# Kernel optimization log

Measured on AMD Instinct MI355X. Metric: run time of the kernel, lower is better.

Reference implementation:

```python
import jax, jax.numpy as jnp
import numpy as np
import math

# dims: batch, in-channels, freq bins, frames(=cropsize), ffn dim, bands
B, C, BINS, W, FF, NB = 16, 8, 1024, 256, 2048, 4
EPS = 1e-5


def _ln(x, g, b):
    m = x.mean(-1, keepdims=True)
    v = ((x - m) ** 2).mean(-1, keepdims=True)
    return (x - m) / jnp.sqrt(v + EPS) * g + b


def _conv1d(x, w, groups=1):
    # x: [b, Cin, L], w: [Cout, Cin//groups, K], 'same' padding
    pad = (w.shape[-1] - 1) // 2
    return jax.lax.conv_general_dilated(
        x, w, (1,), [(pad, pad)],
        dimension_numbers=('NCH', 'OIH', 'NCH'), feature_group_count=groups)


def _mb_attn(x, mem, qw, qb, kw, kb, vw, vb, ow, ob, er, dist_w):
    # MultibandFrameAttention with skewed relative-position bias
    b, w, c = x.shape
    d = c // NB
    q = (x @ qw.T + qb).reshape(b, w, NB, d).transpose(0, 2, 1, 3)    # [b,nb,w,d]
    k = (mem @ kw.T + kb).reshape(b, w, NB, d).transpose(0, 2, 3, 1)  # [b,nb,d,w]
    v = (mem @ vw.T + vb).reshape(b, w, NB, d).transpose(0, 2, 1, 3)  # [b,nb,w,d]
    # skew trick: q @ er -> pad left on last dim -> transpose -> drop first row
    qer = jnp.einsum('bnwd,dc->bnwc', q, er)                           # [b,nb,w,W]
    skew = jnp.pad(qer, ((0, 0), (0, 0), (0, 0), (1, 0)))
    skew = skew.transpose(0, 1, 3, 2)[:, :, 1:, :]                     # [b,nb,W,w]
    idx = jnp.arange(w)
    dist = jnp.abs(idx[:, None] - idx[None, :]).astype(x.dtype) / 2.0  # [w,w]
    p = dist[None] * dist_w + skew                                     # [b,nb,w,w]
    qk = jnp.einsum('bnwd,bndk->bnwk', q, k) / math.sqrt(c)
    a = jax.nn.softmax(qk + p, axis=-1)
    o = jnp.einsum('bnwk,bnkd->bnwd', a, v).transpose(0, 2, 1, 3).reshape(b, w, c)
    return o @ ow.T + ob


def setup_inputs() -> dict:
    key = jax.random.key(0)
    ks = jax.random.split(key, 24)
    rn = lambda k, s, sc=0.02: jax.random.normal(k, s, dtype=jnp.float32) * sc
    d = BINS // NB
    ones = lambda n: jnp.ones((n,), jnp.float32)
    zeros = lambda n: jnp.zeros((n,), jnp.float32)
    return {
        'x': jax.random.normal(ks[0], (B, C, BINS, W), jnp.float32),
        'bott_w': rn(ks[1], (1, C), 0.3),
        'bn_g': ones(1), 'bn_b': zeros(1), 'bn_m': zeros(1), 'bn_v': ones(1),
        'glu_w': rn(ks[2], (2 * BINS, BINS)),
        'n1g': ones(BINS), 'n1b': zeros(BINS),
        'c1L_w': rn(ks[3], (2 * FF, BINS)),
        'c1R_w': rn(ks[4], (FF // 2, BINS, 3)),
        'n2g': ones(2 * FF), 'n2b': zeros(2 * FF),
        'c2dw_w': rn(ks[5], (2 * FF, 1, 9), 0.1),
        'c2pw_w': rn(ks[6], (FF // 2, 2 * FF)),
        'n3g': ones(BINS), 'n3b': zeros(BINS),
        'qw': rn(ks[7], (BINS, BINS)), 'qb': zeros(BINS),
        'kw': rn(ks[8], (BINS, BINS)), 'kb': zeros(BINS),
        'vw': rn(ks[9], (BINS, BINS)), 'vb': zeros(BINS),
        'ow': rn(ks[10], (BINS, BINS)), 'ob': zeros(BINS),
        'er': rn(ks[11], (d, W), 0.02),
        'dist_w': rn(ks[12], (NB, W, 1), 0.02),
        'n4g': ones(BINS), 'n4b': zeros(BINS),
        'c3_w': rn(ks[13], (2 * FF, BINS)),
        'c4_w': rn(ks[14], (BINS, 2 * FF)),
        'n5g': ones(BINS), 'n5b': zeros(BINS),
    }


def reference(x, bott_w, bn_g, bn_b, bn_m, bn_v, glu_w, n1g, n1b,
              c1L_w, c1R_w, n2g, n2b, c2dw_w, c2pw_w, n3g, n3b,
              qw, qb, kw, kb, vw, vb, ow, ob, er, dist_w,
              n4g, n4b, c3_w, c4_w, n5g, n5b):
    # bottleneck: Linear(C->1) over channel dim, BatchNorm2d(1) eval, ReLU
    h0 = jnp.einsum('bchw,oc->bohw', x, bott_w)                        # [b,1,bins,w]
    h0 = (h0 - bn_m[None, :, None, None]) / jnp.sqrt(bn_v[None, :, None, None] + EPS)
    h0 = jax.nn.relu(h0 * bn_g[None, :, None, None] + bn_b[None, :, None, None])
    xs = h0[:, 0].transpose(0, 2, 1)                                   # [b,w,bins]

    # GLU block
    g = xs @ glu_w.T
    a, bgate = g[..., :BINS], g[..., BINS:]
    xs = _ln(xs + a * jax.nn.sigmoid(bgate), n1g, n1b)

    # conv/linear FFN
    hL = jax.nn.relu(xs @ c1L_w.T)                                     # [b,w,2ff]
    hR = jax.nn.relu(_conv1d(xs.transpose(0, 2, 1), c1R_w).transpose(0, 2, 1))
    hR = jnp.pad(hR, ((0, 0), (0, 0), (0, hL.shape[2] - hR.shape[2])))
    h = _ln(hL + hR, n2g, n2b)
    t = _conv1d(h.transpose(0, 2, 1), c2dw_w, groups=2 * FF)           # depthwise
    t = jnp.einsum('bcl,oc->bol', t, c2pw_w).transpose(0, 2, 1)        # [b,w,ff//2]
    t = jnp.pad(t, ((0, 0), (0, 0), (0, xs.shape[2] - t.shape[2])))
    xs = _ln(xs + t, n3g, n3b)

    # multiband attention (self)
    h = _mb_attn(xs, xs, qw, qb, kw, kb, vw, vb, ow, ob, er, dist_w)
    xs = _ln(xs + h, n4g, n4b)

    # final FFN
    h = jax.nn.relu(xs @ c3_w.T) @ c4_w.T
    xs = _ln(xs + h, n5g, n5b)
    return xs.transpose(0, 2, 1)[:, None]                              # [b,1,bins,w]
```

## Files before the change

kernel.cpp:

```cpp
#include <hip/hip_runtime.h>
#include <hip/hip_bf16.h>

#define EPSF 1e-5f

typedef unsigned short u16;
typedef unsigned int   u32;
typedef __attribute__((ext_vector_type(8))) short bf16x8;
typedef __attribute__((ext_vector_type(4))) float f32x4;

__device__ __forceinline__ u16 f2bf(float f) {
    u32 u = __builtin_bit_cast(u32, f);
    u32 r = u + 0x7fffu + ((u >> 16) & 1u);
    return (u16)(r >> 16);
}
__device__ __forceinline__ float bf2f(u16 h) {
    return __builtin_bit_cast(float, (u32)h << 16);
}
__device__ __forceinline__ void gld16(void* lds, const void* gsrc) {
    __builtin_amdgcn_global_load_lds(
        (const __attribute__((address_space(1))) u32*)gsrc,
        (__attribute__((address_space(3))) u32*)lds, 16, 0, 0);
}

__device__ __forceinline__ float wred_sum(float v) {
#pragma unroll
    for (int off = 32; off; off >>= 1) v += __shfl_xor(v, off, 64);
    return v;
}
__device__ __forceinline__ void block_red2(float& s1, float& s2, int tid) {
    __shared__ float red[8];
    s1 = wred_sum(s1); s2 = wred_sum(s2);
    const int lane = tid & 63, wid = tid >> 6;
    if (!lane) { red[wid] = s1; red[4 + wid] = s2; }
    __syncthreads();
    s1 = red[0] + red[1] + red[2] + red[3];
    s2 = red[4] + red[5] + red[6] + red[7];
}

struct Cvt9 { const float* s[9]; u16* d[9]; int n[9]; };
__global__ __launch_bounds__(256)
void wcvt9_k(Cvt9 a)
{
    const int seg = blockIdx.y;
    const int i = blockIdx.x * 256 + threadIdx.x;
    if (i >= a.n[seg]) return;
    const float4 v = ((const float4*)a.s[seg])[i];
    ushort4 o; o.x = f2bf(v.x); o.y = f2bf(v.y); o.z = f2bf(v.z); o.w = f2bf(v.w);
    ((ushort4*)a.d[seg])[i] = o;
}
__global__ __launch_bounds__(256)
void c1rcvt_k(const float* __restrict__ src, u16* __restrict__ dst)
{
    const int i = blockIdx.x * 256 + threadIdx.x;
    const int q = i / 3072, rem = i - q * 3072;
    const int ks = rem >> 10, ci = rem & 1023;
    dst[i] = f2bf(src[((long)q * 1024 + ci) * 3 + ks]);
}
__global__ __launch_bounds__(256)
void ercvt_k(const float* __restrict__ er, u16* __restrict__ erT)
{
    const int i = blockIdx.x * 256 + threadIdx.x;
    const int c = i >> 8, d = i & 255;
    erT[i] = f2bf(er[d * 256 + c]);
}
__global__ __launch_bounds__(256)
void dwcvt_k(const float* __restrict__ src, float* __restrict__ dst)
{
    const int i = blockIdx.x * 256 + threadIdx.x;
    if (i >= 9 * 4096) return;
    const int k = i >> 12, c = i & 4095;
    dst[i] = src[c * 9 + k];
}
__global__ __launch_bounds__(256)
void zero_k(u16* __restrict__ p, int n)
{
    const int i = blockIdx.x * 256 + threadIdx.x;
    if (i < n) p[i] = 0;
}
__global__ __launch_bounds__(256)
void biascat_k(const float* __restrict__ b0, const float* __restrict__ b1,
               const float* __restrict__ b2, float* __restrict__ dst)
{
    const int i = blockIdx.x * 256 + threadIdx.x;
    const float* s = (i < 1024) ? b0 : ((i < 2048) ? b1 : b2);
    dst[i] = s[i & 1023];
}

__global__ __launch_bounds__(256)
void bottleneck_k(const float* __restrict__ x, const float* __restrict__ bw,
                  const float* __restrict__ bn_g, const float* __restrict__ bn_b,
                  const float* __restrict__ bn_m, const float* __restrict__ bn_v,
                  float* __restrict__ xs, u16* __restrict__ xsb)
{
    __shared__ float tile[32][33];
    const int b = blockIdx.z, h0 = blockIdx.y * 32, w0 = blockIdx.x * 32;
    const int tid = threadIdx.x, c = tid & 31, r = tid >> 5;
    float wreg[8];
#pragma unroll
    for (int ch = 0; ch < 8; ++ch) wreg[ch] = bw[ch];
    const float sc = bn_g[0] * rsqrtf(bn_v[0] + EPSF);
    const float sh = bn_b[0] - bn_m[0] * sc;
#pragma unroll
    for (int it = 0; it < 4; ++it) {
        const int h = h0 + r + it * 8;
        const int w = w0 + c;
        float acc = 0.f;
#pragma unroll
        for (int ch = 0; ch < 8; ++ch)
            acc += x[(((long)b * 8 + ch) * 1024 + h) * 256 + w] * wreg[ch];
        tile[r + it * 8][c] = fmaxf(acc * sc + sh, 0.f);
    }
    __syncthreads();
#pragma unroll
    for (int it = 0; it < 4; ++it) {
        const int wl = r + it * 8;
        const float v = tile[c][wl];
        const long o = ((long)b * 256 + w0 + wl) * 1024 + h0 + c;
        xs[o] = v;
        xsb[o] = f2bf(v);
    }
}

template<int ACT, int OUTBF, int BIAS, int SPLITK>
__global__ __launch_bounds__(512, 2)
void gemm8_k(const u16* __restrict__ A, const u16* __restrict__ B,
             const float* __restrict__ bias, void* __restrict__ Cout,
             int N, int K , int lda, int ldb, long partStride)
{
    extern __shared__ u16 lds[];
    const int m0 = blockIdx.y * 256, n0 = blockIdx.x * 256;
    const int koff = (SPLITK > 1) ? blockIdx.z * K : 0;
    const int nt = K >> 6;
    const int tid = threadIdx.x;
    const int lane = tid & 63, wid = tid >> 6;
    const int wr = ((wid >> 2) & 1) * 128;
    const int wc = (wid & 3) * 64;
    const int l15 = lane & 15, l4 = lane >> 4;

    const u16* Ag = A + (long)m0 * lda + koff;
    const u16* Bg = B + (long)n0 * ldb + koff;

    auto stage = [&](const u16* g, int ld, int ldsbase, int kcol, int h) {
#pragma unroll
        for (int is = 0; is < 2; ++is) {
            const int r = h * 128 + is * 64 + (tid >> 3);
            const int sc = ((tid & 7) * 8) ^ (((r >> 2) & 1) << 4);
            gld16(&lds[ldsbase + h * 8192 + is * 4096 + tid * 8],
                  g + (long)r * ld + kcol + sc);
        }
    };
    auto frag = [&](int base, int row, int col) -> bf16x8 {
        return *(const bf16x8*)&lds[base + row * 64 + (col ^ (((row >> 2) & 1) << 4))];
    };

    f32x4 acc[8][4] = {};

    stage(Ag, lda, 0, 0, 0);
    stage(Ag, lda, 0, 0, 1);
    stage(Bg, ldb, 32768, 0, 0);
    stage(Bg, ldb, 32768, 0, 1);
    if (nt > 1) {
        stage(Bg, ldb, 49152, 64, 0);
        stage(Bg, ldb, 49152, 64, 1);
        stage(Ag, lda, 16384, 64, 0);
        asm volatile("s_waitcnt vmcnt(6)" ::: "memory");
    } else {
        asm volatile("s_waitcnt vmcnt(0)" ::: "memory");
    }
    __builtin_amdgcn_s_barrier();

    for (int kt = 0; kt < nt; ++kt) {
        const int cs = kt & 1;
        const int ab = cs * 16384;
        const int bb = 32768 + cs * 16384;
        const int abn = (cs ^ 1) * 16384;
        const int kc1 = (kt + 1) * 64, kc2 = (kt + 2) * 64;
        bf16x8 alo[4][2], ahi[4][2], b01[2][2], b23[2][2];

#pragma unroll
        for (int i = 0; i < 4; ++i)
#pragma unroll
            for (int kk = 0; kk < 2; ++kk)
                alo[i][kk] = frag(ab, wr + i * 16 + l15, kk * 32 + l4 * 8);
#pragma unroll
        for (int j = 0; j < 2; ++j)
#pragma unroll
            for (int kk = 0; kk < 2; ++kk)
                b01[j][kk] = frag(bb, wc + j * 16 + l15, kk * 32 + l4 * 8);
        if (kt + 1 < nt) stage(Ag, lda, abn, kc1, 1);
        __builtin_amdgcn_s_barrier();
        asm volatile("s_waitcnt lgkmcnt(0)" ::: "memory");
        __builtin_amdgcn_s_setprio(1);
#pragma unroll
        for (int i = 0; i < 4; ++i)
#pragma unroll
            for (int j = 0; j < 2; ++j)
#pragma unroll
                for (int kk = 0; kk < 2; ++kk)
                    acc[i][j] = __builtin_amdgcn_mfma_f32_16x16x32_bf16(alo[i][kk], b01[j][kk], acc[i][j], 0, 0, 0);
        __builtin_amdgcn_s_setprio(0);
        __builtin_amdgcn_s_barrier();

#pragma unroll
        for (int j = 0; j < 2; ++j)
#pragma unroll
            for (int kk = 0; kk < 2; ++kk)
                b23[j][kk] = frag(bb, wc + (j + 2) * 16 + l15, kk * 32 + l4 * 8);
        if (kt + 2 < nt) stage(Bg, ldb, bb, kc2, 0);
        __builtin_amdgcn_s_barrier();
        asm volatile("s_waitcnt lgkmcnt(0)" ::: "memory");
        __builtin_amdgcn_s_setprio(1);
#pragma unroll
        for (int i = 0; i < 4; ++i)
#pragma unroll
            for (int j = 0; j < 2; ++j)
#pragma unroll
                for (int kk = 0; kk < 2; ++kk)
                    acc[i][j + 2] = __builtin_amdgcn_mfma_f32_16x16x32_bf16(alo[i][kk], b23[j][kk], acc[i][j + 2], 0, 0, 0);
        __builtin_amdgcn_s_setprio(0);
        __builtin_amdgcn_s_barrier();

#pragma unroll
        for (int i = 0; i < 4; ++i)
#pragma unroll
            for (int kk = 0; kk < 2; ++kk)
                ahi[i][kk] = frag(ab, wr + (i + 4) * 16 + l15, kk * 32 + l4 * 8);
        if (kt + 2 < nt) stage(Bg, ldb, bb, kc2, 1);
        __builtin_amdgcn_s_barrier();
        asm volatile("s_waitcnt lgkmcnt(0)" ::: "memory");
        __builtin_amdgcn_s_setprio(1);
#pragma unroll
        for (int i = 0; i < 4; ++i)
#pragma unroll
            for (int j = 0; j < 2; ++j)
#pragma unroll
                for (int kk = 0; kk < 2; ++kk)
                    acc[i + 4][j + 2] = __builtin_amdgcn_mfma_f32_16x16x32_bf16(ahi[i][kk], b23[j][kk], acc[i + 4][j + 2], 0, 0, 0);
        __builtin_amdgcn_s_setprio(0);
        __builtin_amdgcn_s_barrier();

        if (kt + 2 < nt) stage(Ag, lda, ab, kc2, 0);
        __builtin_amdgcn_s_barrier();
        __builtin_amdgcn_s_setprio(1);
#pragma unroll
        for (int i = 0; i < 4; ++i)
#pragma unroll
            for (int j = 0; j < 2; ++j)
#pragma unroll
                for (int kk = 0; kk < 2; ++kk)
                    acc[i + 4][j] = __builtin_amdgcn_mfma_f32_16x16x32_bf16(ahi[i][kk], b01[j][kk], acc[i + 4][j], 0, 0, 0);
        __builtin_amdgcn_s_setprio(0);
        if (kt + 2 < nt) {
            asm volatile("s_waitcnt vmcnt(6)" ::: "memory");
        } else {
            asm volatile("s_waitcnt vmcnt(0)" ::: "memory");
        }
        __builtin_amdgcn_s_barrier();
    }

    float* Cf = (float*)Cout + ((SPLITK > 1) ? (long)blockIdx.z * partStride : 0);
    u16*   Cb = (u16*)Cout;
#pragma unroll
    for (int i = 0; i < 8; ++i)
#pragma unroll
        for (int j = 0; j < 4; ++j) {
            const int n = n0 + wc + j * 16 + l15;
            const float bv = BIAS ? bias[n] : 0.f;
#pragma unroll
            for (int q = 0; q < 4; ++q) {
                const int m = m0 + wr + i * 16 + l4 * 4 + q;
                float v = acc[i][j][q] + bv;
                if (ACT) v = fmaxf(v, 0.f);
                if (OUTBF) Cb[(long)m * N + n] = f2bf(v);
                else       Cf[(long)m * N + n] = v;
            }
        }
}

__global__ __launch_bounds__(512, 2)
void conv38_k(const u16* __restrict__ Xb, const u16* __restrict__ Wt,
              const u16* __restrict__ zp, float* __restrict__ C)
{
    extern __shared__ u16 lds[];
    const int ks = blockIdx.z;
    const int m0 = blockIdx.y * 256, n0 = blockIdx.x * 256;
    const int nt = 16;
    const int tid = threadIdx.x;
    const int lane = tid & 63, wid = tid >> 6;
    const int wr = ((wid >> 2) & 1) * 128;
    const int wc = (wid & 3) * 64;
    const int l15 = lane & 15, l4 = lane >> 4;

    auto stageA = [&](int ldsbase, int kcol, int h) {
#pragma unroll
        for (int is = 0; is < 2; ++is) {
            const int r = h * 128 + is * 64 + (tid >> 3);
            const int sc = ((tid & 7) * 8) ^ (((r >> 2) & 1) << 4);
            const int t = m0 + r;
            const int wp = (t & 255) + ks - 1;
            const u16* src = ((unsigned)wp < 256u)
                ? Xb + (long)(t + ks - 1) * 1024 + kcol + sc
                : zp;
            gld16(&lds[ldsbase + h * 8192 + is * 4096 + tid * 8], src);
        }
    };
    auto stageB = [&](int ldsbase, int kcol, int h) {
#pragma unroll
        for (int is = 0; is < 2; ++is) {
            const int r = h * 128 + is * 64 + (tid >> 3);
            const int sc = ((tid & 7) * 8) ^ (((r >> 2) & 1) << 4);
            gld16(&lds[ldsbase + h * 8192 + is * 4096 + tid * 8],
                  Wt + (long)(n0 + r) * 3072 + ks * 1024 + kcol + sc);
        }
    };
    auto frag = [&](int base, int row, int col) -> bf16x8 {
        return *(const bf16x8*)&lds[base + row * 64 + (col ^ (((row >> 2) & 1) << 4))];
    };

    f32x4 acc[8][4] = {};

    stageA(0, 0, 0);
    stageA(0, 0, 1);
    stageB(32768, 0, 0);
    stageB(32768, 0, 1);
    stageB(49152, 64, 0);
    stageB(49152, 64, 1);
    stageA(16384, 64, 0);
    asm volatile("s_waitcnt vmcnt(6)" ::: "memory");
    __builtin_amdgcn_s_barrier();

    for (int kt = 0; kt < nt; ++kt) {
        const int cs = kt & 1;
        const int ab = cs * 16384;
        const int bb = 32768 + cs * 16384;
        const int abn = (cs ^ 1) * 16384;
        const int kc1 = (kt + 1) * 64, kc2 = (kt + 2) * 64;
        bf16x8 alo[4][2], ahi[4][2], b01[2][2], b23[2][2];

#pragma unroll
        for (int i = 0; i < 4; ++i)
#pragma unroll
            for (int kk = 0; kk < 2; ++kk)
                alo[i][kk] = frag(ab, wr + i * 16 + l15, kk * 32 + l4 * 8);
#pragma unroll
        for (int j = 0; j < 2; ++j)
#pragma unroll
            for (int kk = 0; kk < 2; ++kk)
                b01[j][kk] = frag(bb, wc + j * 16 + l15, kk * 32 + l4 * 8);
        if (kt + 1 < nt) stageA(abn, kc1, 1);
        __builtin_amdgcn_s_barrier();
        asm volatile("s_waitcnt lgkmcnt(0)" ::: "memory");
        __builtin_amdgcn_s_setprio(1);
#pragma unroll
        for (int i = 0; i < 4; ++i)
#pragma unroll
            for (int j = 0; j < 2; ++j)
#pragma unroll
                for (int kk = 0; kk < 2; ++kk)
                    acc[i][j] = __builtin_amdgcn_mfma_f32_16x16x32_bf16(alo[i][kk], b01[j][kk], acc[i][j], 0, 0, 0);
        __builtin_amdgcn_s_setprio(0);
        __builtin_amdgcn_s_barrier();

#pragma unroll
        for (int j = 0; j < 2; ++j)
#pragma unroll
            for (int kk = 0; kk < 2; ++kk)
                b23[j][kk] = frag(bb, wc + (j + 2) * 16 + l15, kk * 32 + l4 * 8);
        if (kt + 2 < nt) stageB(bb, kc2, 0);
        __builtin_amdgcn_s_barrier();
        asm volatile("s_waitcnt lgkmcnt(0)" ::: "memory");
        __builtin_amdgcn_s_setprio(1);
#pragma unroll
        for (int i = 0; i < 4; ++i)
#pragma unroll
            for (int j = 0; j < 2; ++j)
#pragma unroll
                for (int kk = 0; kk < 2; ++kk)
                    acc[i][j + 2] = __builtin_amdgcn_mfma_f32_16x16x32_bf16(alo[i][kk], b23[j][kk], acc[i][j + 2], 0, 0, 0);
        __builtin_amdgcn_s_setprio(0);
        __builtin_amdgcn_s_barrier();

#pragma unroll
        for (int i = 0; i < 4; ++i)
#pragma unroll
            for (int kk = 0; kk < 2; ++kk)
                ahi[i][kk] = frag(ab, wr + (i + 4) * 16 + l15, kk * 32 + l4 * 8);
        if (kt + 2 < nt) stageB(bb, kc2, 1);
        __builtin_amdgcn_s_barrier();
        asm volatile("s_waitcnt lgkmcnt(0)" ::: "memory");
        __builtin_amdgcn_s_setprio(1);
#pragma unroll
        for (int i = 0; i < 4; ++i)
#pragma unroll
            for (int j = 0; j < 2; ++j)
#pragma unroll
                for (int kk = 0; kk < 2; ++kk)
                    acc[i + 4][j + 2] = __builtin_amdgcn_mfma_f32_16x16x32_bf16(ahi[i][kk], b23[j][kk], acc[i + 4][j + 2], 0, 0, 0);
        __builtin_amdgcn_s_setprio(0);
        __builtin_amdgcn_s_barrier();

        if (kt + 2 < nt) stageA(ab, kc2, 0);
        __builtin_amdgcn_s_barrier();
        __builtin_amdgcn_s_setprio(1);
#pragma unroll
        for (int i = 0; i < 4; ++i)
#pragma unroll
            for (int j = 0; j < 2; ++j)
#pragma unroll
                for (int kk = 0; kk < 2; ++kk)
                    acc[i + 4][j] = __builtin_amdgcn_mfma_f32_16x16x32_bf16(ahi[i][kk], b01[j][kk], acc[i + 4][j], 0, 0, 0);
        __builtin_amdgcn_s_setprio(0);
        if (kt + 2 < nt) {
            asm volatile("s_waitcnt vmcnt(6)" ::: "memory");
        } else {
            asm volatile("s_waitcnt vmcnt(0)" ::: "memory");
        }
        __builtin_amdgcn_s_barrier();
    }

    float* Cp = C + (long)ks * 4194304;
#pragma unroll
    for (int i = 0; i < 8; ++i)
#pragma unroll
        for (int j = 0; j < 4; ++j) {
            const int n = n0 + wc + j * 16 + l15;
#pragma unroll
            for (int q = 0; q < 4; ++q) {
                const int m = m0 + wr + i * 16 + l4 * 4 + q;
                Cp[(long)m * 1024 + n] = acc[i][j][q];
            }
        }
}

__global__ __launch_bounds__(256, 2)
void attn_fused_k(const u16* __restrict__ QKVb, const u16* __restrict__ erT,
                  const u16* __restrict__ Vt, const float* __restrict__ dwp,
                  u16* __restrict__ Oc)
{
    __shared__ __align__(16) u16 As[4096];
    __shared__ __align__(16) u16 Bs[16384];
    __shared__ __align__(16) u16 Pl[16384];
    __shared__ float redM[4][64];
    __shared__ float redS[4][64];
    const int z = blockIdx.y, zb = z >> 2, zn = z & 3;
    const int m0 = blockIdx.x * 64;
    const int tid = threadIdx.x;
    const int lane = tid & 63, wid = tid >> 6;
    const int l15 = lane & 15, l4 = lane >> 4;

    const u16* Qg = QKVb + (long)(zb * 256) * 3072 + zn * 256;
    const u16* Kg = Qg + 1024;

    auto stageA64 = [&](const u16* g, long ld) {
#pragma unroll
        for (int p = 0; p < 2; ++p) {
            const int e = p * 2048 + tid * 8;
            const int r = e >> 6, c = e & 63;
            const int sc = c ^ (((r >> 2) & 1) << 4);
            gld16(&As[e], g + (long)r * ld + sc);
        }
    };
    auto stageB256 = [&](const u16* g, long ld) {
#pragma unroll
        for (int p = 0; p < 8; ++p) {
            const int e = p * 2048 + tid * 8;
            const int r = e >> 6, c = e & 63;
            const int sc = c ^ (((r >> 2) & 1) << 4);
            gld16(&Bs[e], g + (long)r * ld + sc);
        }
    };
    auto fragA = [&](int i, int kk) -> bf16x8 {
        const int row = i * 16 + l15, col = kk * 32 + l4 * 8;
        return *(const bf16x8*)&As[row * 64 + (col ^ (((row >> 2) & 1) << 4))];
    };
    auto fragB = [&](int j, int kk) -> bf16x8 {
        const int row = wid * 64 + j * 16 + l15, col = kk * 32 + l4 * 8;
        return *(const bf16x8*)&Bs[row * 64 + (col ^ (((row >> 2) & 1) << 4))];
    };
    auto fragP = [&](int kc, int i, int kk) -> bf16x8 {
        const int row = i * 16 + l15, col = kk * 32 + l4 * 8;
        return *(const bf16x8*)&Pl[kc * 4096 + row * 64 + (col ^ (((row >> 2) & 1) << 4))];
    };

    f32x4 acc1[4][4] = {};
    f32x4 acc2[4][4] = {};

    for (int kc = 0; kc < 4; ++kc) {
        __syncthreads();
        stageA64(Qg + (long)m0 * 3072 + kc * 64, 3072);
        stageB256(Kg + kc * 64, 3072);
        __syncthreads();
#pragma unroll
        for (int i = 0; i < 4; ++i) {
            const bf16x8 a0 = fragA(i, 0), a1 = fragA(i, 1);
#pragma unroll
            for (int j = 0; j < 4; ++j) {
                acc1[i][j] = __builtin_amdgcn_mfma_f32_16x16x32_bf16(a0, fragB(j, 0), acc1[i][j], 0, 0, 0);
                acc1[i][j] = __builtin_amdgcn_mfma_f32_16x16x32_bf16(a1, fragB(j, 1), acc1[i][j], 0, 0, 0);
            }
        }
    }
    for (int kc = 0; kc < 4; ++kc) {
        __syncthreads();
        stageA64(erT + (long)m0 * 256 + kc * 64, 256);
        stageB256(Qg + kc * 64, 3072);
        __syncthreads();
#pragma unroll
        for (int i = 0; i < 4; ++i) {
            const bf16x8 a0 = fragA(i, 0), a1 = fragA(i, 1);
#pragma unroll
            for (int j = 0; j < 4; ++j) {
                acc2[i][j] = __builtin_amdgcn_mfma_f32_16x16x32_bf16(a0, fragB(j, 0), acc2[i][j], 0, 0, 0);
                acc2[i][j] = __builtin_amdgcn_mfma_f32_16x16x32_bf16(a1, fragB(j, 1), acc2[i][j], 0, 0, 0);
            }
        }
    }

    const float inv32 = 1.f / 32.f;
#pragma unroll
    for (int i = 0; i < 4; ++i)
#pragma unroll
        for (int q = 0; q < 4; ++q) {
            const int mg = m0 + i * 16 + l4 * 4 + q;
            const float dw = dwp[zn * 256 + mg];
#pragma unroll
            for (int j = 0; j < 4; ++j) {
                const int ng = wid * 64 + j * 16 + l15;
                acc1[i][j][q] = acc1[i][j][q] * inv32 + acc2[i][j][q]
                              + fabsf((float)(mg - ng)) * 0.5f * dw;
            }
        }

    float rmax[4][4], rsum[4][4];
#pragma unroll
    for (int i = 0; i < 4; ++i)
#pragma unroll
        for (int q = 0; q < 4; ++q) {
            float mv = fmaxf(fmaxf(acc1[i][0][q], acc1[i][1][q]),
                             fmaxf(acc1[i][2][q], acc1[i][3][q]));
#pragma unroll
            for (int off = 1; off <= 8; off <<= 1) mv = fmaxf(mv, __shfl_xor(mv, off, 64));
            rmax[i][q] = mv;
        }
    if (l15 == 0) {
#pragma unroll
        for (int i = 0; i < 4; ++i)
#pragma unroll
            for (int q = 0; q < 4; ++q)
                redM[wid][i * 16 + l4 * 4 + q] = rmax[i][q];
    }
    __syncthreads();
#pragma unroll
    for (int i = 0; i < 4; ++i)
#pragma unroll
        for (int q = 0; q < 4; ++q) {
            const int ml = i * 16 + l4 * 4 + q;
            rmax[i][q] = fmaxf(fmaxf(redM[0][ml], redM[1][ml]), fmaxf(redM[2][ml], redM[3][ml]));
        }
#pragma unroll
    for (int i = 0; i < 4; ++i)
#pragma unroll
        for (int q = 0; q < 4; ++q) {
            float sv = 0.f;
#pragma unroll
            for (int j = 0; j < 4; ++j) {
                const float e = __expf(acc1[i][j][q] - rmax[i][q]);
                acc1[i][j][q] = e;
                sv += e;
            }
#pragma unroll
            for (int off = 1; off <= 8; off <<= 1) sv += __shfl_xor(sv, off, 64);
            rsum[i][q] = sv;
        }
    if (l15 == 0) {
#pragma unroll
        for (int i = 0; i < 4; ++i)
#pragma unroll
            for (int q = 0; q < 4; ++q)
                redS[wid][i * 16 + l4 * 4 + q] = rsum[i][q];
    }
    __syncthreads();
#pragma unroll
    for (int i = 0; i < 4; ++i)
#pragma unroll
        for (int q = 0; q < 4; ++q) {
            const int ml = i * 16 + l4 * 4 + q;
            rsum[i][q] = redS[0][ml] + redS[1][ml] + redS[2][ml] + redS[3][ml];
        }
#pragma unroll
    for (int i = 0; i < 4; ++i)
#pragma unroll
        for (int q = 0; q < 4; ++q) {
            const float rinv = 1.f / rsum[i][q];
            const int ml = i * 16 + l4 * 4 + q;
#pragma unroll
            for (int j = 0; j < 4; ++j) {
                const int nc = j * 16 + l15;
                Pl[wid * 4096 + ml * 64 + (nc ^ (((ml >> 2) & 1) << 4))] = f2bf(acc1[i][j][q] * rinv);
            }
        }
    __syncthreads();

    f32x4 accO[4][4] = {};
    for (int kc = 0; kc < 4; ++kc) {
        __syncthreads();
        stageB256(Vt + (long)(z * 256) * 256 + kc * 64, 256);
        __syncthreads();
#pragma unroll
        for (int i = 0; i < 4; ++i) {
            const bf16x8 a0 = fragP(kc, i, 0), a1 = fragP(kc, i, 1);
#pragma unroll
            for (int j = 0; j < 4; ++j) {
                accO[i][j] = __builtin_amdgcn_mfma_f32_16x16x32_bf16(a0, fragB(j, 0), accO[i][j], 0, 0, 0);
                accO[i][j] = __builtin_amdgcn_mfma_f32_16x16x32_bf16(a1, fragB(j, 1), accO[i][j], 0, 0, 0);
            }
        }
    }

#pragma unroll
    for (int i = 0; i < 4; ++i)
#pragma unroll
        for (int j = 0; j < 4; ++j) {
            const int d = wid * 64 + j * 16 + l15;
#pragma unroll
            for (int q = 0; q < 4; ++q) {
                const int mg = m0 + i * 16 + l4 * 4 + q;
                Oc[(long)(zb * 256 + mg) * 1024 + zn * 256 + d] = f2bf(accO[i][j][q]);
            }
        }
}

__global__ __launch_bounds__(256)
void glu_ln_k(const float* __restrict__ xs0, const float* __restrict__ g2,
              const float* __restrict__ gam, const float* __restrict__ bet,
              float* __restrict__ outf, u16* __restrict__ outb)
{
    const int t = blockIdx.x, tid = threadIdx.x;
    const int f0 = tid * 4;
    const long PS = 8388608;
    const float4 xv = *(const float4*)&xs0[(long)t * 1024 + f0];
    float4 av = *(const float4*)&g2[(long)t * 2048 + f0];
    float4 gv = *(const float4*)&g2[(long)t * 2048 + 1024 + f0];
    const float4 av1 = *(const float4*)&g2[PS + (long)t * 2048 + f0];
    const float4 gv1 = *(const float4*)&g2[PS + (long)t * 2048 + 1024 + f0];
    av.x += av1.x; av.y += av1.y; av.z += av1.z; av.w += av1.w;
    gv.x += gv1.x; gv.y += gv1.y; gv.z += gv1.z; gv.w += gv1.w;
    float vals[4];
    vals[0] = xv.x + av.x / (1.f + expf(-gv.x));
    vals[1] = xv.y + av.y / (1.f + expf(-gv.y));
    vals[2] = xv.z + av.z / (1.f + expf(-gv.z));
    vals[3] = xv.w + av.w / (1.f + expf(-gv.w));
    float s1 = vals[0] + vals[1] + vals[2] + vals[3];
    float s2 = vals[0]*vals[0] + vals[1]*vals[1] + vals[2]*vals[2] + vals[3]*vals[3];
    block_red2(s1, s2, tid);
    const float mean = s1 * (1.f / 1024.f);
    const float var  = s2 * (1.f / 1024.f) - mean * mean;
    const float rstd = rsqrtf(var + EPSF);
    const float4 gm = *(const float4*)&gam[f0];
    const float4 bt = *(const float4*)&bet[f0];
    float r0 = (vals[0] - mean) * rstd * gm.x + bt.x;
    float r1 = (vals[1] - mean) * rstd * gm.y + bt.y;
    float r2 = (vals[2] - mean) * rstd * gm.z + bt.z;
    float r3 = (vals[3] - mean) * rstd * gm.w + bt.w;
    *(float4*)&outf[(long)t * 1024 + f0] = make_float4(r0, r1, r2, r3);
    ushort4 ub; ub.x = f2bf(r0); ub.y = f2bf(r1); ub.z = f2bf(r2); ub.w = f2bf(r3);
    *(ushort4*)&outb[(long)t * 1024 + f0] = ub;
}

template<int P, int WRITEBF, int BIAS>
__global__ __launch_bounds__(256)
void add_ln1024_k(const float* __restrict__ A, const float* __restrict__ Bp,
                  const float* __restrict__ bias,
                  const float* __restrict__ gam, const float* __restrict__ bet,
                  float* __restrict__ outf, u16* __restrict__ outb)
{
    const int t = blockIdx.x, tid = threadIdx.x;
    const int f0 = tid * 4;
    const long PS = 4194304;
    const float4 a = *(const float4*)&A[(long)t * 1024 + f0];
    float4 b = *(const float4*)&Bp[(long)t * 1024 + f0];
#pragma unroll
    for (int p = 1; p < P; ++p) {
        const float4 bp = *(const float4*)&Bp[p * PS + (long)t * 1024 + f0];
        b.x += bp.x; b.y += bp.y; b.z += bp.z; b.w += bp.w;
    }
    if (BIAS) {
        const float4 bb = *(const float4*)&bias[f0];
        b.x += bb.x; b.y += bb.y; b.z += bb.z; b.w += bb.w;
    }
    float vals[4] = {a.x + b.x, a.y + b.y, a.z + b.z, a.w + b.w};
    float s1 = vals[0] + vals[1] + vals[2] + vals[3];
    float s2 = vals[0]*vals[0] + vals[1]*vals[1] + vals[2]*vals[2] + vals[3]*vals[3];
    block_red2(s1, s2, tid);
    const float mean = s1 * (1.f / 1024.f);
    const float var  = s2 * (1.f / 1024.f) - mean * mean;
    const float rstd = rsqrtf(var + EPSF);
    const float4 gm = *(const float4*)&gam[f0];
    const float4 bt = *(const float4*)&bet[f0];
    float r0 = (vals[0] - mean) * rstd * gm.x + bt.x;
    float r1 = (vals[1] - mean) * rstd * gm.y + bt.y;
    float r2 = (vals[2] - mean) * rstd * gm.z + bt.z;
    float r3 = (vals[3] - mean) * rstd * gm.w + bt.w;
    *(float4*)&outf[(long)t * 1024 + f0] = make_float4(r0, r1, r2, r3);
    if (WRITEBF) {
        ushort4 ub; ub.x = f2bf(r0); ub.y = f2bf(r1); ub.z = f2bf(r2); ub.w = f2bf(r3);
        *(ushort4*)&outb[(long)t * 1024 + f0] = ub;
    }
}

__global__ __launch_bounds__(256)
void add_ln4096_k(const u16* __restrict__ A, const float* __restrict__ Bp,
                  const float* __restrict__ gam, const float* __restrict__ bet,
                  u16* __restrict__ outb)
{
    const int t = blockIdx.x, tid = threadIdx.x;
    const long PS = 4194304;
    const int f0 = tid * 16;
    float vals[16];
    const bf16x8 a0 = *(const bf16x8*)&A[(long)t * 4096 + f0];
    const bf16x8 a1 = *(const bf16x8*)&A[(long)t * 4096 + f0 + 8];
#pragma unroll
    for (int e = 0; e < 8; ++e) { vals[e] = bf2f((u16)a0[e]); vals[8 + e] = bf2f((u16)a1[e]); }
    if (tid < 64) {
#pragma unroll
        for (int c = 0; c < 4; ++c) {
            const int fc = f0 + c * 4;
            float4 b  = *(const float4*)&Bp[(long)t * 1024 + fc];
            const float4 b1 = *(const float4*)&Bp[PS + (long)t * 1024 + fc];
            const float4 b2 = *(const float4*)&Bp[2 * PS + (long)t * 1024 + fc];
            vals[c*4+0] += fmaxf(b.x + b1.x + b2.x, 0.f);
            vals[c*4+1] += fmaxf(b.y + b1.y + b2.y, 0.f);
            vals[c*4+2] += fmaxf(b.z + b1.z + b2.z, 0.f);
            vals[c*4+3] += fmaxf(b.w + b1.w + b2.w, 0.f);
        }
    }
    float s1 = 0.f, s2 = 0.f;
#pragma unroll
    for (int e = 0; e < 16; ++e) { s1 += vals[e]; s2 += vals[e] * vals[e]; }
    block_red2(s1, s2, tid);
    const float mean = s1 * (1.f / 4096.f);
    const float var  = s2 * (1.f / 4096.f) - mean * mean;
    const float rstd = rsqrtf(var + EPSF);
#pragma unroll
    for (int c = 0; c < 4; ++c) {
        const int fc = f0 + c * 4;
        const float4 gm = *(const float4*)&gam[fc];
        const float4 bt = *(const float4*)&bet[fc];
        ushort4 ub;
        ub.x = f2bf((vals[c*4+0] - mean) * rstd * gm.x + bt.x);
        ub.y = f2bf((vals[c*4+1] - mean) * rstd * gm.y + bt.y);
        ub.z = f2bf((vals[c*4+2] - mean) * rstd * gm.z + bt.z);
        ub.w = f2bf((vals[c*4+3] - mean) * rstd * gm.w + bt.w);
        *(ushort4*)&outb[(long)t * 4096 + fc] = ub;
    }
}

__global__ __launch_bounds__(256)
void dwconv8_k(const u16* __restrict__ h, const float* __restrict__ wT,
               u16* __restrict__ out)
{
    const long idx = (long)blockIdx.x * 256 + threadIdx.x;
    const int cg = (int)(idx & 511);
    const int t  = (int)(idx >> 9);
    const int w  = t & 255;
    const int c0 = cg * 8;
    float acc[8] = {};
#pragma unroll
    for (int k = 0; k < 9; ++k) {
        const int wp = w + k - 4;
        if ((unsigned)wp < 256u) {
            const bf16x8 hv = *(const bf16x8*)&h[(long)(t + k - 4) * 4096 + c0];
            const float4 w0 = *(const float4*)&wT[k * 4096 + c0];
            const float4 w1 = *(const float4*)&wT[k * 4096 + c0 + 4];
            acc[0] += bf2f((u16)hv[0]) * w0.x;
            acc[1] += bf2f((u16)hv[1]) * w0.y;
            acc[2] += bf2f((u16)hv[2]) * w0.z;
            acc[3] += bf2f((u16)hv[3]) * w0.w;
            acc[4] += bf2f((u16)hv[4]) * w1.x;
            acc[5] += bf2f((u16)hv[5]) * w1.y;
            acc[6] += bf2f((u16)hv[6]) * w1.z;
            acc[7] += bf2f((u16)hv[7]) * w1.w;
        }
    }
    bf16x8 res;
#pragma unroll
    for (int j = 0; j < 8; ++j) res[j] = (short)f2bf(acc[j]);
    *(bf16x8*)&out[(long)t * 4096 + c0] = res;
}

__global__ __launch_bounds__(256)
void vtrans_k(const u16* __restrict__ QKVb, u16* __restrict__ Vt)
{
    __shared__ u16 t[32][33];
    const int z = blockIdx.z, zb = z >> 2, zn = z & 3;
    const int w0 = blockIdx.x * 32, d0 = blockIdx.y * 32;
    const int tid = threadIdx.x, c = tid & 31, r = tid >> 5;
#pragma unroll
    for (int it = 0; it < 4; ++it) {
        const int wl = r + it * 8;
        t[wl][c] = QKVb[(long)(zb * 256 + w0 + wl) * 3072 + 2048 + zn * 256 + d0 + c];
    }
    __syncthreads();
#pragma unroll
    for (int it = 0; it < 4; ++it) {
        const int dl = r + it * 8;
        Vt[((long)z * 256 + d0 + dl) * 256 + w0 + c] = t[c][dl];
    }
}

__global__ __launch_bounds__(256)
void transpose_out_k(const float* __restrict__ xs, float* __restrict__ out)
{
    __shared__ float tile[32][33];
    const int b = blockIdx.z, f0 = blockIdx.y * 32, w0 = blockIdx.x * 32;
    const int tid = threadIdx.x, c = tid & 31, r = tid >> 5;
#pragma unroll
    for (int it = 0; it < 4; ++it) {
        const int w = w0 + r + it * 8;
        tile[r + it * 8][c] = xs[((long)b * 256 + w) * 1024 + f0 + c];
    }
    __syncthreads();
#pragma unroll
    for (int it = 0; it < 4; ++it) {
        const int fl = r + it * 8;
        out[((long)b * 1024 + f0 + fl) * 256 + w0 + c] = tile[c][fl];
    }
}

extern "C" void kernel_launch(void* const* d_in, const int* in_sizes, int n_in,
                              void* d_out, int out_size, void* d_ws, size_t ws_size,
                              hipStream_t stream)
{
    const float* x      = (const float*)d_in[0];
    const float* bott_w = (const float*)d_in[1];
    const float* bn_g   = (const float*)d_in[2];
    const float* bn_b   = (const float*)d_in[3];
    const float* bn_m   = (const float*)d_in[4];
    const float* bn_v   = (const float*)d_in[5];
    const float* glu_w  = (const float*)d_in[6];
    const float* n1g    = (const float*)d_in[7];
    const float* n1b    = (const float*)d_in[8];
    const float* c1L_w  = (const float*)d_in[9];
    const float* c1R_w  = (const float*)d_in[10];
    const float* n2g    = (const float*)d_in[11];
    const float* n2b    = (const float*)d_in[12];
    const float* c2dw_w = (const float*)d_in[13];
    const float* c2pw_w = (const float*)d_in[14];
    const float* n3g    = (const float*)d_in[15];
    const float* n3b    = (const float*)d_in[16];
    const float* qw     = (const float*)d_in[17];
    const float* qb     = (const float*)d_in[18];
    const float* kw     = (const float*)d_in[19];
    const float* kb     = (const float*)d_in[20];
    const float* vw     = (const float*)d_in[21];
    const float* vb     = (const float*)d_in[22];
    const float* ow     = (const float*)d_in[23];
    const float* ob     = (const float*)d_in[24];
    const float* er     = (const float*)d_in[25];
    const float* dist_w = (const float*)d_in[26];
    const float* n4g    = (const float*)d_in[27];
    const float* n4b    = (const float*)d_in[28];
    const float* c3_w   = (const float*)d_in[29];
    const float* c4_w   = (const float*)d_in[30];
    const float* n5g    = (const float*)d_in[31];
    const float* n5b    = (const float*)d_in[32];
    float* out = (float*)d_out;

    char* Wb_ = (char*)d_ws;
    auto F  = [&](size_t mib) { return (float*)(Wb_ + (mib << 20)); };
    auto Bf = [&](size_t mib) { return (u16*)  (Wb_ + (mib << 20)); };
    float* X0   = F(0);
    float* X1   = F(16);
    u16*   H0b  = Bf(32);
    float* Hglu = F(64);
    float* C3p  = F(64);
    float* P4   = F(64);
    u16*   H1b  = Bf(128);
    u16*   Hdw  = Bf(160);
    u16*   QKVb = Bf(192);
    u16*   Vt   = Bf(216);
    u16*   S1b  = Bf(264);
    u16*   XbA  = Bf(280);
    u16*   XbB  = Bf(288);
    u16* wGLU = Bf(296); u16* wC1L = Bf(300); u16* wC1R = Bf(308);
    u16* wC2P = Bf(314); u16* wQKV = Bf(322); u16* wO   = Bf(328);
    u16* wC3  = Bf(330); u16* wC4  = Bf(338);
    u16* erT  = Bf(346);
    u16* zp   = (u16*)(Wb_ + (346u << 20) + 131072);
    float* wdwT = (float*)(Wb_ + (346u << 20) + 131072 + 16384);
    float* bQKV = (float*)(Wb_ + (346u << 20) + 131072 + 16384 + 147456);

    const dim3 blk(256);
    const dim3 blk8(512);
    const long PS1 = 4194304;
    const size_t SH8 = 131072;

    zero_k<<<dim3(32), blk, 0, stream>>>(zp, 8192);
    Cvt9 cv;
    cv.s[0] = glu_w;  cv.d[0] = wGLU;            cv.n[0] = 524288;
    cv.s[1] = c1L_w;  cv.d[1] = wC1L;            cv.n[1] = 1048576;
    cv.s[2] = c2pw_w; cv.d[2] = wC2P;            cv.n[2] = 1048576;
    cv.s[3] = c3_w;   cv.d[3] = wC3;             cv.n[3] = 1048576;
    cv.s[4] = c4_w;   cv.d[4] = wC4;             cv.n[4] = 1048576;
    cv.s[5] = qw;     cv.d[5] = wQKV;            cv.n[5] = 262144;
    cv.s[6] = kw;     cv.d[6] = wQKV + 1048576;  cv.n[6] = 262144;
    cv.s[7] = vw;     cv.d[7] = wQKV + 2097152;  cv.n[7] = 262144;
    cv.s[8] = ow;     cv.d[8] = wO;              cv.n[8] = 262144;
    wcvt9_k<<<dim3(4096, 9), blk, 0, stream>>>(cv);
    c1rcvt_k<<<dim3(12288), blk, 0, stream>>>(c1R_w, wC1R);
    ercvt_k<<<dim3(256), blk, 0, stream>>>(er, erT);
    dwcvt_k<<<dim3(144), blk, 0, stream>>>(c2dw_w, wdwT);
    biascat_k<<<dim3(12), blk, 0, stream>>>(qb, kb, vb, bQKV);

    bottleneck_k<<<dim3(8, 32, 16), blk, 0, stream>>>(x, bott_w, bn_g, bn_b, bn_m, bn_v, X1, XbA);

    gemm8_k<0,0,0,2><<<dim3(8, 16, 2), blk8, SH8, stream>>>(XbA, wGLU, nullptr, Hglu,
        2048, 512, 1024, 1024, (long)4096 * 2048);

    glu_ln_k<<<dim3(4096), blk, 0, stream>>>(X1, Hglu, n1g, n1b, X0, XbB);

    gemm8_k<1,1,0,1><<<dim3(16, 16, 1), blk8, SH8, stream>>>(XbB, wC1L, nullptr, H0b,
        4096, 1024, 1024, 1024, 0);

    conv38_k<<<dim3(4, 16, 3), blk8, SH8, stream>>>(XbB, wC1R, zp, C3p);

    add_ln4096_k<<<dim3(4096), blk, 0, stream>>>(H0b, C3p, n2g, n2b, H1b);

    dwconv8_k<<<dim3(8192), blk, 0, stream>>>(H1b, wdwT, Hdw);

    gemm8_k<0,0,0,4><<<dim3(4, 16, 4), blk8, SH8, stream>>>(Hdw, wC2P, nullptr, P4,
        1024, 1024, 4096, 4096, PS1);

    add_ln1024_k<4,1,0><<<dim3(4096), blk, 0, stream>>>(X0, P4, nullptr, n3g, n3b, X1, XbA);

    gemm8_k<0,1,1,1><<<dim3(12, 16, 1), blk8, SH8, stream>>>(XbA, wQKV, bQKV, QKVb,
        3072, 1024, 1024, 1024, 0);

    vtrans_k<<<dim3(8, 8, 64), blk, 0, stream>>>(QKVb, Vt);

    attn_fused_k<<<dim3(4, 64), blk, 0, stream>>>(QKVb, erT, Vt, dist_w, S1b);

    gemm8_k<0,0,0,4><<<dim3(4, 16, 4), blk8, SH8, stream>>>(S1b, wO, nullptr, P4,
        1024, 256, 1024, 1024, PS1);

    add_ln1024_k<4,1,1><<<dim3(4096), blk, 0, stream>>>(X1, P4, ob, n4g, n4b, X0, XbB);

    gemm8_k<1,1,0,1><<<dim3(16, 16, 1), blk8, SH8, stream>>>(XbB, wC3, nullptr, H0b,
        4096, 1024, 1024, 1024, 0);

    gemm8_k<0,0,0,4><<<dim3(4, 16, 4), blk8, SH8, stream>>>(H0b, wC4, nullptr, P4,
        1024, 1024, 4096, 4096, PS1);

    add_ln1024_k<4,0,0><<<dim3(4096), blk, 0, stream>>>(X0, P4, nullptr, n5g, n5b, X1, nullptr);

    transpose_out_k<<<dim3(8, 32, 16), blk, 0, stream>>>(X1, out);

    (void)in_sizes; (void)n_in; (void)out_size; (void)ws_size;
}
```

Baseline: 553.8 us.

## Store split-K partials in bf16 and merge setup conversion kernels into one launch

Split-K GEMM and conv38 partial outputs are now written as bf16 instead of fp32. The reducing LayerNorm kernels read them back with ushort4 loads and convert to float, which halves partial-buffer traffic. The six weight-prep and zeroing kernels are also merged into one setup_k launch with segment offsets, saving launch overhead and trimming wasted blocks in the 9x4096 grid. The cost is extra rounding on partial sums before they are summed.

```diff
diff --git a/kernel.cpp b/kernel.cpp
--- a/kernel.cpp
+++ b/kernel.cpp
@@ -15,6 +15,9 @@
 }
 __device__ __forceinline__ float bf2f(u16 h) {
     return __builtin_bit_cast(float, (u32)h << 16);
+}
+__device__ __forceinline__ float4 bf4f(ushort4 v) {
+    return make_float4(bf2f(v.x), bf2f(v.y), bf2f(v.z), bf2f(v.w));
 }
 __device__ __forceinline__ void gld16(void* lds, const void* gsrc) {
     __builtin_amdgcn_global_load_lds(
@@ -37,53 +40,43 @@
     s2 = red[4] + red[5] + red[6] + red[7];
 }
 
-struct Cvt9 { const float* s[9]; u16* d[9]; int n[9]; };
+struct SetupArgs {
+    const float* ws[9]; u16* wd[9]; int wn[9];
+    const float* c1r; u16* c1rd;
+    const float* er;  u16* erd;
+    const float* dw;  float* dwd;
+    const float* qb;  const float* kb; const float* vb; float* bcat;
+    u16* zp;
+    int off[15];
+};
 __global__ __launch_bounds__(256)
-void wcvt9_k(Cvt9 a)
-{
-    const int seg = blockIdx.y;
-    const int i = blockIdx.x * 256 + threadIdx.x;
-    if (i >= a.n[seg]) return;
-    const float4 v = ((const float4*)a.s[seg])[i];
-    ushort4 o; o.x = f2bf(v.x); o.y = f2bf(v.y); o.z = f2bf(v.z); o.w = f2bf(v.w);
-    ((ushort4*)a.d[seg])[i] = o;
-}
-__global__ __launch_bounds__(256)
-void c1rcvt_k(const float* __restrict__ src, u16* __restrict__ dst)
-{
-    const int i = blockIdx.x * 256 + threadIdx.x;
-    const int q = i / 3072, rem = i - q * 3072;
-    const int ks = rem >> 10, ci = rem & 1023;
-    dst[i] = f2bf(src[((long)q * 1024 + ci) * 3 + ks]);
-}
-__global__ __launch_bounds__(256)
-void ercvt_k(const float* __restrict__ er, u16* __restrict__ erT)
-{
-    const int i = blockIdx.x * 256 + threadIdx.x;
-    const int c = i >> 8, d = i & 255;
-    erT[i] = f2bf(er[d * 256 + c]);
-}
-__global__ __launch_bounds__(256)
-void dwcvt_k(const float* __restrict__ src, float* __restrict__ dst)
-{
-    const int i = blockIdx.x * 256 + threadIdx.x;
-    if (i >= 9 * 4096) return;
-    const int k = i >> 12, c = i & 4095;
-    dst[i] = src[c * 9 + k];
-}
-__global__ __launch_bounds__(256)
-void zero_k(u16* __restrict__ p, int n)
-{
-    const int i = blockIdx.x * 256 + threadIdx.x;
-    if (i < n) p[i] = 0;
-}
-__global__ __launch_bounds__(256)
-void biascat_k(const float* __restrict__ b0, const float* __restrict__ b1,
-               const float* __restrict__ b2, float* __restrict__ dst)
-{
-    const int i = blockIdx.x * 256 + threadIdx.x;
-    const float* s = (i < 1024) ? b0 : ((i < 2048) ? b1 : b2);
-    dst[i] = s[i & 1023];
+void setup_k(SetupArgs a)
+{
+    const int b = blockIdx.x;
+    int seg = 0;
+    while (seg < 13 && b >= a.off[seg + 1]) ++seg;
+    const int i = (b - a.off[seg]) * 256 + threadIdx.x;
+    if (seg < 9) {
+        if (i < a.wn[seg]) {
+            const float4 v = ((const float4*)a.ws[seg])[i];
+            ushort4 o; o.x = f2bf(v.x); o.y = f2bf(v.y); o.z = f2bf(v.z); o.w = f2bf(v.w);
+            ((ushort4*)a.wd[seg])[i] = o;
+        }
+    } else if (seg == 9) {
+        if (i < 3145728) {
+            const int q = i / 3072, rem = i - q * 3072;
+            const int ks = rem >> 10, ci = rem & 1023;
+            a.c1rd[i] = f2bf(a.c1r[((long)q * 1024 + ci) * 3 + ks]);
+        }
+    } else if (seg == 10) {
+        if (i < 65536) { const int c = i >> 8, d = i & 255; a.erd[i] = f2bf(a.er[d * 256 + c]); }
+    } else if (seg == 11) {
+        if (i < 36864) { const int k = i >> 12, c = i & 4095; a.dwd[i] = a.dw[c * 9 + k]; }
+    } else if (seg == 12) {
+        if (i < 3072) { const float* s = (i < 1024) ? a.qb : ((i < 2048) ? a.kb : a.vb); a.bcat[i] = s[i & 1023]; }
+    } else {
+        if (i < 8192) a.zp[i] = 0;
+    }
 }
 
 __global__ __launch_bounds__(256)
@@ -258,28 +251,43 @@
         __builtin_amdgcn_s_barrier();
     }
 
-    float* Cf = (float*)Cout + ((SPLITK > 1) ? (long)blockIdx.z * partStride : 0);
-    u16*   Cb = (u16*)Cout;
-#pragma unroll
-    for (int i = 0; i < 8; ++i)
-#pragma unroll
-        for (int j = 0; j < 4; ++j) {
-            const int n = n0 + wc + j * 16 + l15;
-            const float bv = BIAS ? bias[n] : 0.f;
-#pragma unroll
-            for (int q = 0; q < 4; ++q) {
-                const int m = m0 + wr + i * 16 + l4 * 4 + q;
-                float v = acc[i][j][q] + bv;
-                if (ACT) v = fmaxf(v, 0.f);
-                if (OUTBF) Cb[(long)m * N + n] = f2bf(v);
-                else       Cf[(long)m * N + n] = v;
+    if (SPLITK > 1) {
+        u16* Cp = (u16*)Cout + (long)blockIdx.z * partStride;
+#pragma unroll
+        for (int i = 0; i < 8; ++i)
+#pragma unroll
+            for (int j = 0; j < 4; ++j) {
+                const int n = n0 + wc + j * 16 + l15;
+#pragma unroll
+                for (int q = 0; q < 4; ++q) {
+                    const int m = m0 + wr + i * 16 + l4 * 4 + q;
+                    Cp[(long)m * N + n] = f2bf(acc[i][j][q]);
+                }
             }
-        }
+    } else {
+        float* Cf = (float*)Cout;
+        u16*   Cb = (u16*)Cout;
+#pragma unroll
+        for (int i = 0; i < 8; ++i)
+#pragma unroll
+            for (int j = 0; j < 4; ++j) {
+                const int n = n0 + wc + j * 16 + l15;
+                const float bv = BIAS ? bias[n] : 0.f;
+#pragma unroll
+                for (int q = 0; q < 4; ++q) {
+                    const int m = m0 + wr + i * 16 + l4 * 4 + q;
+                    float v = acc[i][j][q] + bv;
+                    if (ACT) v = fmaxf(v, 0.f);
+                    if (OUTBF) Cb[(long)m * N + n] = f2bf(v);
+                    else       Cf[(long)m * N + n] = v;
+                }
+            }
+    }
 }
 
 __global__ __launch_bounds__(512, 2)
 void conv38_k(const u16* __restrict__ Xb, const u16* __restrict__ Wt,
-              const u16* __restrict__ zp, float* __restrict__ C)
+              const u16* __restrict__ zp, u16* __restrict__ C)
 {
     extern __shared__ u16 lds[];
     const int ks = blockIdx.z;
@@ -418,7 +426,7 @@
         __builtin_amdgcn_s_barrier();
     }
 
-    float* Cp = C + (long)ks * 4194304;
+    u16* Cp = C + (long)ks * 4194304;
 #pragma unroll
     for (int i = 0; i < 8; ++i)
 #pragma unroll
@@ -427,7 +435,7 @@
 #pragma unroll
             for (int q = 0; q < 4; ++q) {
                 const int m = m0 + wr + i * 16 + l4 * 4 + q;
-                Cp[(long)m * 1024 + n] = acc[i][j][q];
+                Cp[(long)m * 1024 + n] = f2bf(acc[i][j][q]);
             }
         }
 }
@@ -631,7 +639,7 @@
 }
 
 __global__ __launch_bounds__(256)
-void glu_ln_k(const float* __restrict__ xs0, const float* __restrict__ g2,
+void glu_ln_k(const float* __restrict__ xs0, const u16* __restrict__ g2,
               const float* __restrict__ gam, const float* __restrict__ bet,
               float* __restrict__ outf, u16* __restrict__ outb)
 {
@@ -639,17 +647,17 @@
     const int f0 = tid * 4;
     const long PS = 8388608;
     const float4 xv = *(const float4*)&xs0[(long)t * 1024 + f0];
-    float4 av = *(const float4*)&g2[(long)t * 2048 + f0];
-    float4 gv = *(const float4*)&g2[(long)t * 2048 + 1024 + f0];
-    const float4 av1 = *(const float4*)&g2[PS + (long)t * 2048 + f0];
-    const float4 gv1 = *(const float4*)&g2[PS + (long)t * 2048 + 1024 + f0];
-    av.x += av1.x; av.y += av1.y; av.z += av1.z; av.w += av1.w;
-    gv.x += gv1.x; gv.y += gv1.y; gv.z += gv1.z; gv.w += gv1.w;
+    const float4 a0 = bf4f(*(const ushort4*)&g2[(long)t * 2048 + f0]);
+    const float4 g0 = bf4f(*(const ushort4*)&g2[(long)t * 2048 + 1024 + f0]);
+    const float4 a1 = bf4f(*(const ushort4*)&g2[PS + (long)t * 2048 + f0]);
+    const float4 g1 = bf4f(*(const ushort4*)&g2[PS + (long)t * 2048 + 1024 + f0]);
+    const float ax = a0.x + a1.x, ay = a0.y + a1.y, az = a0.z + a1.z, aw = a0.w + a1.w;
+    const float gx = g0.x + g1.x, gy = g0.y + g1.y, gz = g0.z + g1.z, gw = g0.w + g1.w;
     float vals[4];
-    vals[0] = xv.x + av.x / (1.f + expf(-gv.x));
-    vals[1] = xv.y + av.y / (1.f + expf(-gv.y));
-    vals[2] = xv.z + av.z / (1.f + expf(-gv.z));
-    vals[3] = xv.w + av.w / (1.f + expf(-gv.w));
+    vals[0] = xv.x + ax / (1.f + expf(-gx));
+    vals[1] = xv.y + ay / (1.f + expf(-gy));
+    vals[2] = xv.z + az / (1.f + expf(-gz));
+    vals[3] = xv.w + aw / (1.f + expf(-gw));
     float s1 = vals[0] + vals[1] + vals[2] + vals[3];
     float s2 = vals[0]*vals[0] + vals[1]*vals[1] + vals[2]*vals[2] + vals[3]*vals[3];
     block_red2(s1, s2, tid);
@@ -669,7 +677,7 @@
 
 template<int P, int WRITEBF, int BIAS>
 __global__ __launch_bounds__(256)
-void add_ln1024_k(const float* __restrict__ A, const float* __restrict__ Bp,
+void add_ln1024_k(const float* __restrict__ A, const u16* __restrict__ Bp,
                   const float* __restrict__ bias,
                   const float* __restrict__ gam, const float* __restrict__ bet,
                   float* __restrict__ outf, u16* __restrict__ outb)
@@ -678,10 +686,10 @@
     const int f0 = tid * 4;
     const long PS = 4194304;
     const float4 a = *(const float4*)&A[(long)t * 1024 + f0];
-    float4 b = *(const float4*)&Bp[(long)t * 1024 + f0];
+    float4 b = bf4f(*(const ushort4*)&Bp[(long)t * 1024 + f0]);
 #pragma unroll
     for (int p = 1; p < P; ++p) {
-        const float4 bp = *(const float4*)&Bp[p * PS + (long)t * 1024 + f0];
+        const float4 bp = bf4f(*(const ushort4*)&Bp[p * PS + (long)t * 1024 + f0]);
         b.x += bp.x; b.y += bp.y; b.z += bp.z; b.w += bp.w;
     }
     if (BIAS) {
@@ -709,7 +717,7 @@
 }
 
 __global__ __launch_bounds__(256)
-void add_ln4096_k(const u16* __restrict__ A, const float* __restrict__ Bp,
+void add_ln4096_k(const u16* __restrict__ A, const u16* __restrict__ Bp,
                   const float* __restrict__ gam, const float* __restrict__ bet,
                   u16* __restrict__ outb)
 {
@@ -725,13 +733,13 @@
 #pragma unroll
         for (int c = 0; c < 4; ++c) {
             const int fc = f0 + c * 4;
-            float4 b  = *(const float4*)&Bp[(long)t * 1024 + fc];
-            const float4 b1 = *(const float4*)&Bp[PS + (long)t * 1024 + fc];
-            const float4 b2 = *(const float4*)&Bp[2 * PS + (long)t * 1024 + fc];
-            vals[c*4+0] += fmaxf(b.x + b1.x + b2.x, 0.f);
-            vals[c*4+1] += fmaxf(b.y + b1.y + b2.y, 0.f);
-            vals[c*4+2] += fmaxf(b.z + b1.z + b2.z, 0.f);
-            vals[c*4+3] += fmaxf(b.w + b1.w + b2.w, 0.f);
+            const float4 b0 = bf4f(*(const ushort4*)&Bp[(long)t * 1024 + fc]);
+            const float4 b1 = bf4f(*(const ushort4*)&Bp[PS + (long)t * 1024 + fc]);
+            const float4 b2 = bf4f(*(const ushort4*)&Bp[2 * PS + (long)t * 1024 + fc]);
+            vals[c*4+0] += fmaxf(b0.x + b1.x + b2.x, 0.f);
+            vals[c*4+1] += fmaxf(b0.y + b1.y + b2.y, 0.f);
+            vals[c*4+2] += fmaxf(b0.z + b1.z + b2.z, 0.f);
+            vals[c*4+3] += fmaxf(b0.w + b1.w + b2.w, 0.f);
         }
     }
     float s1 = 0.f, s2 = 0.f;
@@ -872,9 +880,9 @@
     float* X0   = F(0);
     float* X1   = F(16);
     u16*   H0b  = Bf(32);
-    float* Hglu = F(64);
-    float* C3p  = F(64);
-    float* P4   = F(64);
+    u16*   Hglu = Bf(64);
+    u16*   C3p  = Bf(64);
+    u16*   P4   = Bf(64);
     u16*   H1b  = Bf(128);
     u16*   Hdw  = Bf(160);
     u16*   QKVb = Bf(192);
@@ -895,22 +903,29 @@
     const long PS1 = 4194304;
     const size_t SH8 = 131072;
 
-    zero_k<<<dim3(32), blk, 0, stream>>>(zp, 8192);
-    Cvt9 cv;
-    cv.s[0] = glu_w;  cv.d[0] = wGLU;            cv.n[0] = 524288;
-    cv.s[1] = c1L_w;  cv.d[1] = wC1L;            cv.n[1] = 1048576;
-    cv.s[2] = c2pw_w; cv.d[2] = wC2P;            cv.n[2] = 1048576;
-    cv.s[3] = c3_w;   cv.d[3] = wC3;             cv.n[3] = 1048576;
-    cv.s[4] = c4_w;   cv.d[4] = wC4;             cv.n[4] = 1048576;
-    cv.s[5] = qw;     cv.d[5] = wQKV;            cv.n[5] = 262144;
-    cv.s[6] = kw;     cv.d[6] = wQKV + 1048576;  cv.n[6] = 262144;
-    cv.s[7] = vw;     cv.d[7] = wQKV + 2097152;  cv.n[7] = 262144;
-    cv.s[8] = ow;     cv.d[8] = wO;              cv.n[8] = 262144;
-    wcvt9_k<<<dim3(4096, 9), blk, 0, stream>>>(cv);
-    c1rcvt_k<<<dim3(12288), blk, 0, stream>>>(c1R_w, wC1R);
-    ercvt_k<<<dim3(256), blk, 0, stream>>>(er, erT);
-    dwcvt_k<<<dim3(144), blk, 0, stream>>>(c2dw_w, wdwT);
-    biascat_k<<<dim3(12), blk, 0, stream>>>(qb, kb, vb, bQKV);
+    SetupArgs sa;
+    sa.ws[0] = glu_w;  sa.wd[0] = wGLU;            sa.wn[0] = 524288;
+    sa.ws[1] = c1L_w;  sa.wd[1] = wC1L;            sa.wn[1] = 1048576;
+    sa.ws[2] = c2pw_w; sa.wd[2] = wC2P;            sa.wn[2] = 1048576;
+    sa.ws[3] = c3_w;   sa.wd[3] = wC3;             sa.wn[3] = 1048576;
+    sa.ws[4] = c4_w;   sa.wd[4] = wC4;             sa.wn[4] = 1048576;
+    sa.ws[5] = qw;     sa.wd[5] = wQKV;            sa.wn[5] = 262144;
+    sa.ws[6] = kw;     sa.wd[6] = wQKV + 1048576;  sa.wn[6] = 262144;
+    sa.ws[7] = vw;     sa.wd[7] = wQKV + 2097152;  sa.wn[7] = 262144;
+    sa.ws[8] = ow;     sa.wd[8] = wO;              sa.wn[8] = 262144;
+    sa.c1r = c1R_w; sa.c1rd = wC1R;
+    sa.er  = er;    sa.erd  = erT;
+    sa.dw  = c2dw_w; sa.dwd = wdwT;
+    sa.qb = qb; sa.kb = kb; sa.vb = vb; sa.bcat = bQKV;
+    sa.zp = zp;
+    {
+        int bc[14] = {2048, 4096, 4096, 4096, 4096, 1024, 1024, 1024, 1024,
+                      12288, 256, 144, 12, 32};
+        int acc = 0;
+        for (int s = 0; s < 14; ++s) { sa.off[s] = acc; acc += bc[s]; }
+        sa.off[14] = acc;
+        setup_k<<<dim3(acc), blk, 0, stream>>>(sa);
+    }
 
     bottleneck_k<<<dim3(8, 32, 16), blk, 0, stream>>>(x, bott_w, bn_g, bn_b, bn_m, bn_v, X1, XbA);
 
```

Result: faster. 512.7 us (-7.4%).
